# Optimization experiments

Hardware: AMD Instinct MI355X
Metric: run time of the kernel (lower is better)

Reference implementation:

```python
import jax, jax.numpy as jnp
import numpy as np

N_ITER = 2  # args.n_iter; aggregator = 'sum'


def setup_inputs() -> dict:
    key = jax.random.key(0)
    B, D, S = 8192, 128, 16
    NUM_USER, NUM_ENT, NUM_REL = 100000, 500000, 64
    ks = jax.random.split(key, 9)
    return {
        "u": jax.random.randint(ks[0], (B,), 0, NUM_USER),
        "v": jax.random.randint(ks[1], (B,), 0, NUM_ENT),
        "adj_ent": jax.random.randint(ks[2], (NUM_ENT, S), 0, NUM_ENT),
        "adj_rel": jax.random.randint(ks[3], (NUM_ENT, S), 0, NUM_REL),
        "usr_table": jax.random.normal(ks[4], (NUM_USER, D), jnp.float32) * 0.1,
        "ent_table": jax.random.normal(ks[5], (NUM_ENT, D), jnp.float32) * 0.1,
        "rel_table": jax.random.normal(ks[6], (NUM_REL, D), jnp.float32) * 0.1,
        "W": jax.random.normal(ks[7], (D, D), jnp.float32) * (1.0 / np.sqrt(D)),
        "b": jnp.zeros((D,), jnp.float32),
    }


def reference(u, v, adj_ent, adj_rel, usr_table, ent_table, rel_table, W, b):
    # NOTE: in the original code, _message_passing always reads base entity
    # embeddings for neighbors, so the neighbor message is identical at every
    # hop and the output depends only on v's own adjacency row.
    u_emb = usr_table[u]                              # [B, D]
    nbr_emb = ent_table[adj_ent[v]]                   # [B, S, D] gather
    rel_emb = rel_table[adj_rel[v]]                   # [B, S, D] gather
    scores = jnp.einsum('bd,bsd->bs', u_emb, rel_emb)  # pi_{u,r}
    attn = jax.nn.softmax(scores, axis=-1)            # softmax over S neighbors
    msg = jnp.einsum('bs,bsd->bd', attn, nbr_emb)     # weighted neighbor sum
    rep = ent_table[v]                                # rep^0 = ent(v)
    for _ in range(N_ITER):                           # 'sum' aggregator, eq.4
        rep = jax.nn.relu((msg + rep) @ W + b)
    return jax.nn.sigmoid(jnp.sum(u_emb * rep, axis=1))  # [B]
```

## Files before the change

### kernel.cpp

```cpp
#include <hip/hip_runtime.h>

#define D 128
#define S 16

__global__ __launch_bounds__(256) void k1_attn(
    const int* __restrict__ u, const int* __restrict__ v,
    const int* __restrict__ adj_ent, const int* __restrict__ adj_rel,
    const float* __restrict__ usr, const float* __restrict__ ent,
    const float* __restrict__ rel, float* __restrict__ msg_out)
{
    const int tid  = threadIdx.x;
    const int grp  = tid >> 5;
    const int lane = tid & 31;
    const int b    = blockIdx.x * 8 + grp;

    const int uu = u[b];
    const int vv = v[b];

    const float4 u4 = *(const float4*)(usr + (size_t)uu * D + lane * 4);

    const int ae = adj_ent[(size_t)vv * S + (lane & 15)];
    const int ar = adj_rel[(size_t)vv * S + (lane & 15)];

    float sc[S];
    #pragma unroll
    for (int h = 0; h < 2; ++h) {
        float4 r4[8];
        #pragma unroll
        for (int s = 0; s < 8; ++s) {
            const int nr = __shfl(ar, h * 8 + s, 32);
            r4[s] = *(const float4*)(rel + (size_t)nr * D + lane * 4);
        }
        #pragma unroll
        for (int s = 0; s < 8; ++s) {
            float p = u4.x * r4[s].x + u4.y * r4[s].y +
                      u4.z * r4[s].z + u4.w * r4[s].w;
            #pragma unroll
            for (int off = 16; off >= 1; off >>= 1) p += __shfl_xor(p, off, 32);
            sc[h * 8 + s] = p;
        }
    }

    float mx = sc[0];
    #pragma unroll
    for (int s = 1; s < S; ++s) mx = fmaxf(mx, sc[s]);
    float sum = 0.f;
    #pragma unroll
    for (int s = 0; s < S; ++s) { sc[s] = __expf(sc[s] - mx); sum += sc[s]; }
    const float inv = 1.f / sum;

    float m0 = 0.f, m1 = 0.f, m2 = 0.f, m3 = 0.f;
    #pragma unroll
    for (int h = 0; h < 2; ++h) {
        float4 n4[8];
        #pragma unroll
        for (int s = 0; s < 8; ++s) {
            const int ne = __shfl(ae, h * 8 + s, 32);
            n4[s] = *(const float4*)(ent + (size_t)ne * D + lane * 4);
        }
        #pragma unroll
        for (int s = 0; s < 8; ++s) {
            const float a = sc[h * 8 + s] * inv;
            m0 += a * n4[s].x; m1 += a * n4[s].y;
            m2 += a * n4[s].z; m3 += a * n4[s].w;
        }
    }
    *(float4*)(msg_out + (size_t)b * D + lane * 4) = make_float4(m0, m1, m2, m3);
}

__global__ __launch_bounds__(256) void k2_layers(
    const int* __restrict__ u, const int* __restrict__ v,
    const float* __restrict__ usr, const float* __restrict__ ent,
    const float* __restrict__ W, const float* __restrict__ bias,
    const float* __restrict__ msg_in, float* __restrict__ out)
{
    __shared__ float sMsg[16 * D];
    __shared__ float sX[16 * D];
    __shared__ float sR[16 * D];

    const int tid = threadIdx.x;
    const int b0  = blockIdx.x * 16;

    {
        const float4* src = (const float4*)(msg_in + (size_t)b0 * D);
        float4* dst = (float4*)sMsg;
        #pragma unroll
        for (int k = 0; k < 2; ++k) dst[k * 256 + tid] = src[k * 256 + tid];
    }
    {
        const int grp = tid >> 5, lane = tid & 31;
        #pragma unroll
        for (int p = 0; p < 2; ++p) {
            const int e  = p * 8 + grp;
            const int vv = v[b0 + e];
            *(float4*)&sR[e * D + lane * 4] =
                *(const float4*)(ent + (size_t)vv * D + lane * 4);
        }
    }
    __syncthreads();

    const int mg = tid >> 5, jg = tid & 31;
    const int m0 = mg * 2, j0 = jg * 4;
    float bf[4];
    #pragma unroll
    for (int c = 0; c < 4; ++c) bf[c] = bias[j0 + c];

    for (int it = 0; it < 2; ++it) {
        #pragma unroll
        for (int k = 0; k < 8; ++k) {
            const int idx = k * 256 + tid;
            sX[idx] = sMsg[idx] + sR[idx];
        }
        __syncthreads();

        float acc[2][4];
        #pragma unroll
        for (int k = 0; k < 2; ++k)
            #pragma unroll
            for (int c = 0; c < 4; ++c) acc[k][c] = 0.f;

        #pragma unroll 4
        for (int d = 0; d < D; ++d) {
            const float4 w4 = *(const float4*)(W + d * D + j0);
            #pragma unroll
            for (int k = 0; k < 2; ++k) {
                const float xm = sX[(m0 + k) * D + d];
                acc[k][0] += xm * w4.x; acc[k][1] += xm * w4.y;
                acc[k][2] += xm * w4.z; acc[k][3] += xm * w4.w;
            }
        }

        #pragma unroll
        for (int k = 0; k < 2; ++k) {
            float4 y;
            y.x = fmaxf(acc[k][0] + bf[0], 0.f);
            y.y = fmaxf(acc[k][1] + bf[1], 0.f);
            y.z = fmaxf(acc[k][2] + bf[2], 0.f);
            y.w = fmaxf(acc[k][3] + bf[3], 0.f);
            *(float4*)&sR[(m0 + k) * D + j0] = y;
        }
        __syncthreads();
    }

    #pragma unroll
    for (int p = 0; p < 2; ++p) {
        const int e  = p * 8 + mg;
        const int bb = b0 + e;
        const int uu = u[bb];
        const float4 u4 = *(const float4*)(usr + (size_t)uu * D + jg * 4);
        const float4 rf = *(const float4*)&sR[e * D + jg * 4];
        float pr = u4.x * rf.x + u4.y * rf.y + u4.z * rf.z + u4.w * rf.w;
        #pragma unroll
        for (int off = 16; off >= 1; off >>= 1) pr += __shfl_xor(pr, off, 32);
        if (jg == 0) out[bb] = 1.f / (1.f + __expf(-pr));
    }
}

extern "C" void kernel_launch(void* const* d_in, const int* in_sizes, int n_in,
                              void* d_out, int out_size, void* d_ws, size_t ws_size,
                              hipStream_t stream)
{
    const int* u       = (const int*)d_in[0];
    const int* v       = (const int*)d_in[1];
    const int* adj_ent = (const int*)d_in[2];
    const int* adj_rel = (const int*)d_in[3];
    const float* usr   = (const float*)d_in[4];
    const float* ent   = (const float*)d_in[5];
    const float* rel   = (const float*)d_in[6];
    const float* W     = (const float*)d_in[7];
    const float* bias  = (const float*)d_in[8];

    float* msg_ws = (float*)d_ws;
    float* out = (float*)d_out;

    hipLaunchKernelGGL(k1_attn, dim3(8192 / 8), dim3(256), 0, stream,
                       u, v, adj_ent, adj_rel, usr, ent, rel, msg_ws);
    hipLaunchKernelGGL(k2_layers, dim3(8192 / 16), dim3(256), 0, stream,
                       u, v, usr, ent, W, bias, msg_ws, out);
}
```

Before: 385.4 us.

## Fuse attention and dense layers into one kernel with earlier neighbor gathers

Merges the attention/message kernel and the two-layer dense kernel into a single launch. The message stays in registers and shared memory instead of going through a global workspace, which removes a kernel launch and the msg write/read round trip. The neighbor-embedding gathers are also issued earlier, interleaved with the relation gathers, to overlap memory latency. In exchange, each block now runs only 8 rows through the W matmul instead of 16, so W reuse per block drops, and the larger set of live float4 arrays raises register pressure.

```diff
diff --git a/kernel.cpp b/kernel.cpp
--- a/kernel.cpp
+++ b/kernel.cpp
@@ -3,12 +3,15 @@
 #define D 128
 #define S 16
 
-__global__ __launch_bounds__(256) void k1_attn(
+__global__ __launch_bounds__(256) void kgcn_fused(
     const int* __restrict__ u, const int* __restrict__ v,
     const int* __restrict__ adj_ent, const int* __restrict__ adj_rel,
     const float* __restrict__ usr, const float* __restrict__ ent,
-    const float* __restrict__ rel, float* __restrict__ msg_out)
+    const float* __restrict__ rel, const float* __restrict__ W,
+    const float* __restrict__ bias, float* __restrict__ out)
 {
+    __shared__ float sX[8 * D];
+
     const int tid  = threadIdx.x;
     const int grp  = tid >> 5;
     const int lane = tid & 31;
@@ -17,28 +20,45 @@
     const int uu = u[b];
     const int vv = v[b];
 
-    const float4 u4 = *(const float4*)(usr + (size_t)uu * D + lane * 4);
+    const float4 u4   = *(const float4*)(usr + (size_t)uu * D + lane * 4);
+    const float4 rep0 = *(const float4*)(ent + (size_t)vv * D + lane * 4);
 
     const int ae = adj_ent[(size_t)vv * S + (lane & 15)];
     const int ar = adj_rel[(size_t)vv * S + (lane & 15)];
 
     float sc[S];
+    float4 r4[8], n4a[8], n4b[8];
+
     #pragma unroll
-    for (int h = 0; h < 2; ++h) {
-        float4 r4[8];
+    for (int s = 0; s < 8; ++s) {
+        const int nr = __shfl(ar, s, 32);
+        r4[s] = *(const float4*)(rel + (size_t)nr * D + lane * 4);
+    }
+    #pragma unroll
+    for (int s = 0; s < 8; ++s) {
+        const int ne = __shfl(ae, s, 32);
+        n4a[s] = *(const float4*)(ent + (size_t)ne * D + lane * 4);
+    }
+    #pragma unroll
+    for (int s = 0; s < 8; ++s) {
+        float p = u4.x * r4[s].x + u4.y * r4[s].y +
+                  u4.z * r4[s].z + u4.w * r4[s].w;
         #pragma unroll
-        for (int s = 0; s < 8; ++s) {
-            const int nr = __shfl(ar, h * 8 + s, 32);
-            r4[s] = *(const float4*)(rel + (size_t)nr * D + lane * 4);
-        }
+        for (int off = 16; off >= 1; off >>= 1) p += __shfl_xor(p, off, 32);
+        sc[s] = p;
+    }
+    #pragma unroll
+    for (int s = 0; s < 8; ++s) {
+        const int nr = __shfl(ar, 8 + s, 32);
+        r4[s] = *(const float4*)(rel + (size_t)nr * D + lane * 4);
+    }
+    #pragma unroll
+    for (int s = 0; s < 8; ++s) {
+        float p = u4.x * r4[s].x + u4.y * r4[s].y +
+                  u4.z * r4[s].z + u4.w * r4[s].w;
         #pragma unroll
-        for (int s = 0; s < 8; ++s) {
-            float p = u4.x * r4[s].x + u4.y * r4[s].y +
-                      u4.z * r4[s].z + u4.w * r4[s].w;
-            #pragma unroll
-            for (int off = 16; off >= 1; off >>= 1) p += __shfl_xor(p, off, 32);
-            sc[h * 8 + s] = p;
-        }
+        for (int off = 16; off >= 1; off >>= 1) p += __shfl_xor(p, off, 32);
+        sc[8 + s] = p;
     }
 
     float mx = sc[0];
@@ -49,111 +69,74 @@
     for (int s = 0; s < S; ++s) { sc[s] = __expf(sc[s] - mx); sum += sc[s]; }
     const float inv = 1.f / sum;
 
+    #pragma unroll
+    for (int s = 0; s < 8; ++s) {
+        const int ne = __shfl(ae, 8 + s, 32);
+        n4b[s] = *(const float4*)(ent + (size_t)ne * D + lane * 4);
+    }
+
     float m0 = 0.f, m1 = 0.f, m2 = 0.f, m3 = 0.f;
     #pragma unroll
-    for (int h = 0; h < 2; ++h) {
-        float4 n4[8];
-        #pragma unroll
-        for (int s = 0; s < 8; ++s) {
-            const int ne = __shfl(ae, h * 8 + s, 32);
-            n4[s] = *(const float4*)(ent + (size_t)ne * D + lane * 4);
+    for (int s = 0; s < 8; ++s) {
+        const float a = sc[s] * inv;
+        m0 += a * n4a[s].x; m1 += a * n4a[s].y;
+        m2 += a * n4a[s].z; m3 += a * n4a[s].w;
+    }
+    #pragma unroll
+    for (int s = 0; s < 8; ++s) {
+        const float a = sc[8 + s] * inv;
+        m0 += a * n4b[s].x; m1 += a * n4b[s].y;
+        m2 += a * n4b[s].z; m3 += a * n4b[s].w;
+    }
+
+    const int j0 = lane * 4;
+    const float4 b4 = *(const float4*)(bias + j0);
+    const float* xrow = &sX[grp * D];
+
+    *(float4*)&sX[grp * D + j0] =
+        make_float4(m0 + rep0.x, m1 + rep0.y, m2 + rep0.z, m3 + rep0.w);
+    __syncthreads();
+
+    float4 y;
+    {
+        float a0 = 0.f, a1 = 0.f, a2 = 0.f, a3 = 0.f;
+        #pragma unroll 4
+        for (int d = 0; d < D; ++d) {
+            const float4 w4 = *(const float4*)(W + d * D + j0);
+            const float xm = xrow[d];
+            a0 += xm * w4.x; a1 += xm * w4.y;
+            a2 += xm * w4.z; a3 += xm * w4.w;
         }
-        #pragma unroll
-        for (int s = 0; s < 8; ++s) {
-            const float a = sc[h * 8 + s] * inv;
-            m0 += a * n4[s].x; m1 += a * n4[s].y;
-            m2 += a * n4[s].z; m3 += a * n4[s].w;
-        }
-    }
-    *(float4*)(msg_out + (size_t)b * D + lane * 4) = make_float4(m0, m1, m2, m3);
-}
-
-__global__ __launch_bounds__(256) void k2_layers(
-    const int* __restrict__ u, const int* __restrict__ v,
-    const float* __restrict__ usr, const float* __restrict__ ent,
-    const float* __restrict__ W, const float* __restrict__ bias,
-    const float* __restrict__ msg_in, float* __restrict__ out)
-{
-    __shared__ float sMsg[16 * D];
-    __shared__ float sX[16 * D];
-    __shared__ float sR[16 * D];
-
-    const int tid = threadIdx.x;
-    const int b0  = blockIdx.x * 16;
-
-    {
-        const float4* src = (const float4*)(msg_in + (size_t)b0 * D);
-        float4* dst = (float4*)sMsg;
-        #pragma unroll
-        for (int k = 0; k < 2; ++k) dst[k * 256 + tid] = src[k * 256 + tid];
-    }
-    {
-        const int grp = tid >> 5, lane = tid & 31;
-        #pragma unroll
-        for (int p = 0; p < 2; ++p) {
-            const int e  = p * 8 + grp;
-            const int vv = v[b0 + e];
-            *(float4*)&sR[e * D + lane * 4] =
-                *(const float4*)(ent + (size_t)vv * D + lane * 4);
-        }
+        y.x = fmaxf(a0 + b4.x, 0.f);
+        y.y = fmaxf(a1 + b4.y, 0.f);
+        y.z = fmaxf(a2 + b4.z, 0.f);
+        y.w = fmaxf(a3 + b4.w, 0.f);
     }
     __syncthreads();
 
-    const int mg = tid >> 5, jg = tid & 31;
-    const int m0 = mg * 2, j0 = jg * 4;
-    float bf[4];
-    #pragma unroll
-    for (int c = 0; c < 4; ++c) bf[c] = bias[j0 + c];
+    *(float4*)&sX[grp * D + j0] =
+        make_float4(m0 + y.x, m1 + y.y, m2 + y.z, m3 + y.w);
+    __syncthreads();
 
-    for (int it = 0; it < 2; ++it) {
-        #pragma unroll
-        for (int k = 0; k < 8; ++k) {
-            const int idx = k * 256 + tid;
-            sX[idx] = sMsg[idx] + sR[idx];
-        }
-        __syncthreads();
-
-        float acc[2][4];
-        #pragma unroll
-        for (int k = 0; k < 2; ++k)
-            #pragma unroll
-            for (int c = 0; c < 4; ++c) acc[k][c] = 0.f;
-
+    {
+        float a0 = 0.f, a1 = 0.f, a2 = 0.f, a3 = 0.f;
         #pragma unroll 4
         for (int d = 0; d < D; ++d) {
             const float4 w4 = *(const float4*)(W + d * D + j0);
-            #pragma unroll
-            for (int k = 0; k < 2; ++k) {
-                const float xm = sX[(m0 + k) * D + d];
-                acc[k][0] += xm * w4.x; acc[k][1] += xm * w4.y;
-                acc[k][2] += xm * w4.z; acc[k][3] += xm * w4.w;
-            }
+            const float xm = xrow[d];
+            a0 += xm * w4.x; a1 += xm * w4.y;
+            a2 += xm * w4.z; a3 += xm * w4.w;
         }
-
-        #pragma unroll
-        for (int k = 0; k < 2; ++k) {
-            float4 y;
-            y.x = fmaxf(acc[k][0] + bf[0], 0.f);
-            y.y = fmaxf(acc[k][1] + bf[1], 0.f);
-            y.z = fmaxf(acc[k][2] + bf[2], 0.f);
-            y.w = fmaxf(acc[k][3] + bf[3], 0.f);
-            *(float4*)&sR[(m0 + k) * D + j0] = y;
-        }
-        __syncthreads();
+        y.x = fmaxf(a0 + b4.x, 0.f);
+        y.y = fmaxf(a1 + b4.y, 0.f);
+        y.z = fmaxf(a2 + b4.z, 0.f);
+        y.w = fmaxf(a3 + b4.w, 0.f);
     }
 
+    float pr = u4.x * y.x + u4.y * y.y + u4.z * y.z + u4.w * y.w;
     #pragma unroll
-    for (int p = 0; p < 2; ++p) {
-        const int e  = p * 8 + mg;
-        const int bb = b0 + e;
-        const int uu = u[bb];
-        const float4 u4 = *(const float4*)(usr + (size_t)uu * D + jg * 4);
-        const float4 rf = *(const float4*)&sR[e * D + jg * 4];
-        float pr = u4.x * rf.x + u4.y * rf.y + u4.z * rf.z + u4.w * rf.w;
-        #pragma unroll
-        for (int off = 16; off >= 1; off >>= 1) pr += __shfl_xor(pr, off, 32);
-        if (jg == 0) out[bb] = 1.f / (1.f + __expf(-pr));
-    }
+    for (int off = 16; off >= 1; off >>= 1) pr += __shfl_xor(pr, off, 32);
+    if (lane == 0) out[b] = 1.f / (1.f + __expf(-pr));
 }
 
 extern "C" void kernel_launch(void* const* d_in, const int* in_sizes, int n_in,
@@ -169,12 +152,8 @@
     const float* rel   = (const float*)d_in[6];
     const float* W     = (const float*)d_in[7];
     const float* bias  = (const float*)d_in[8];
-
-    float* msg_ws = (float*)d_ws;
     float* out = (float*)d_out;
 
-    hipLaunchKernelGGL(k1_attn, dim3(8192 / 8), dim3(256), 0, stream,
-                       u, v, adj_ent, adj_rel, usr, ent, rel, msg_ws);
-    hipLaunchKernelGGL(k2_layers, dim3(8192 / 16), dim3(256), 0, stream,
-                       u, v, usr, ent, W, bias, msg_ws, out);
+    hipLaunchKernelGGL(kgcn_fused, dim3(8192 / 8), dim3(256), 0, stream,
+                       u, v, adj_ent, adj_rel, usr, ent, rel, W, bias, out);
 }
```

Measured after the change: 386.2 us. No clear change (+0.2%).
